# Performance work log

Hardware: AMD Instinct MI355X
Metric: run time of the kernel (lower is better)

The kernel has to match this reference:

```python
import jax, jax.numpy as jnp
import numpy as np

N = 50000        # nodes
E = 400000       # edges (no self-loops; self-loops appended in forward)
IN_DIM = 128
H, C = 4, 64     # heads, channels per head
D = H * C        # 256
NEG_SLOPE = 0.2


def setup_inputs() -> dict:
    key = jax.random.key(0)
    ks = jax.random.split(key, 8)
    x = jax.random.normal(ks[0], (N, IN_DIM), jnp.float32)
    # build edges with no self-loops (src != dst), matching the module's mask
    src = jax.random.randint(ks[1], (E,), 0, N)
    off = jax.random.randint(ks[2], (E,), 1, N)
    dst = (src + off) % N
    edge_index = jnp.stack([src, dst]).astype(jnp.int32)
    inp = {"x": x, "edge_index": edge_index}
    dims_in = [IN_DIM, D, D, D, D]
    for l in range(5):
        k = jax.random.split(ks[3 + l], 4)
        inp[f"W{l}"] = jax.random.normal(k[0], (D, dims_in[l]), jnp.float32) * 0.05
        inp[f"att_src{l}"] = jax.random.normal(k[1], (1, H, C), jnp.float32) * 0.05
        inp[f"att_dst{l}"] = jax.random.normal(k[2], (1, H, C), jnp.float32) * 0.05
        inp[f"bias{l}"] = jnp.zeros((D,), jnp.float32)
    return inp


def _gat_layer(x, W, a_src, a_dst, b, src, dst, relu_out):
    # linear projection, reshape to [N, H, C]
    h = (x @ W.T).reshape(N, H, C)
    alpha_src = jnp.sum(h * a_src, axis=-1)   # [N, H]
    alpha_dst = jnp.sum(h * a_dst, axis=-1)   # [N, H]
    # per-edge logits: alpha_j (source) + alpha_i (dest)
    alpha = jax.nn.leaky_relu(alpha_src[src] + alpha_dst[dst], negative_slope=NEG_SLOPE)  # [E', H]
    # segment softmax over destination neighborhoods (max is detached, as in the original)
    m = jax.lax.stop_gradient(jax.ops.segment_max(alpha, dst, num_segments=N))  # [N, H]
    e = jnp.exp(alpha - m[dst])
    s = jax.ops.segment_sum(e, dst, num_segments=N) + 1e-16
    a = e / s[dst]                                                             # [E', H]
    # weighted scatter-add aggregation of gathered source features
    out = jax.ops.segment_sum(a[:, :, None] * h[src], dst, num_segments=N)     # [N, H, C]
    out = out.reshape(N, D) + b
    return jax.nn.relu(out) if relu_out else out


def reference(x, edge_index,
              W0, att_src0, att_dst0, bias0,
              W1, att_src1, att_dst1, bias1,
              W2, att_src2, att_dst2, bias2,
              W3, att_src3, att_dst3, bias3,
              W4, att_src4, att_dst4, bias4):
    # input edges contain no self-loops; append one self-loop per node (as in the trace)
    loops = jnp.arange(N, dtype=edge_index.dtype)
    src = jnp.concatenate([edge_index[0], loops])
    dst = jnp.concatenate([edge_index[1], loops])
    params = [(W0, att_src0, att_dst0, bias0), (W1, att_src1, att_dst1, bias1),
              (W2, att_src2, att_dst2, bias2), (W3, att_src3, att_dst3, bias3),
              (W4, att_src4, att_dst4, bias4)]
    h = x
    for l, (W, a_s, a_d, b) in enumerate(params):
        h = _gat_layer(h, W, a_s, a_d, b, src, dst, relu_out=(l < 4))
    return h
```

## Files before the change

### kernel.cpp

```cpp
#include <hip/hip_runtime.h>
#include <hip/hip_bf16.h>

#define H 4
#define D 256
#define NEG_SLOPE 0.2f

typedef __attribute__((ext_vector_type(8))) _Float16 f16x8;
typedef __attribute__((ext_vector_type(4))) _Float16 f16x4;
typedef __attribute__((ext_vector_type(4))) float f32x4;

__global__ void k_cvt_all(const float* __restrict__ x,
                          const float* __restrict__ w0, const float* __restrict__ w1,
                          const float* __restrict__ w2, const float* __restrict__ w3,
                          const float* __restrict__ w4,
                          _Float16* __restrict__ xf, _Float16* __restrict__ wf,
                          int nx4) {
    int i = blockIdx.x * blockDim.x + threadIdx.x;
    const int nW0 = 128 * 256 / 4, nW = 256 * 256 / 4;
    const float* src;
    _Float16* dst;
    int off;
    if (i < nx4) { src = x; dst = xf; off = i; }
    else {
        i -= nx4;
        if (i < nW0) { src = w0; dst = wf; off = i; }
        else {
            i -= nW0;
            int l = i / nW, r2 = i % nW;
            if (l >= 4) return;
            const float* ws[4] = {w1, w2, w3, w4};
            src = ws[l];
            dst = wf + 128 * 256 + (size_t)l * 256 * 256;
            off = r2;
        }
    }
    float4 v = ((const float4*)src)[off];
    f16x4 o = {(_Float16)v.x, (_Float16)v.y, (_Float16)v.z, (_Float16)v.w};
    *(f16x4*)&dst[(size_t)off * 4] = o;
}

template<int K>
__global__ __launch_bounds__(256) void k_gemm_mfma(
        const _Float16* __restrict__ xf, const _Float16* __restrict__ wf,
        const float* __restrict__ att_src, const float* __restrict__ att_dst,
        _Float16* __restrict__ hmat, float* __restrict__ alpha_src,
        float* __restrict__ alpha_dst, int nrows) {
    __shared__ _Float16 sx[64][40];
    __shared__ _Float16 sw[256][40];
    int t = threadIdx.x;
    int w = t >> 6, l = t & 63;
    int r = l & 15, q = l >> 4;
    int row0 = blockIdx.x * 64;
    f32x4 acc[16];
    #pragma unroll
    for (int cf = 0; cf < 16; ++cf) acc[cf] = (f32x4){0.f, 0.f, 0.f, 0.f};

    for (int k0 = 0; k0 < K; k0 += 32) {
        __syncthreads();
        {
            int gr = row0 + (t >> 2);
            uint4 v = make_uint4(0, 0, 0, 0);
            if (gr < nrows) v = *(const uint4*)&xf[(size_t)gr * K + k0 + (t & 3) * 8];
            *(uint4*)&sx[t >> 2][(t & 3) * 8] = v;
        }
        #pragma unroll
        for (int i = 0; i < 4; ++i) {
            int wr = (t >> 2) + i * 64;
            uint4 v = *(const uint4*)&wf[(size_t)wr * K + k0 + (t & 3) * 8];
            *(uint4*)&sw[wr][(t & 3) * 8] = v;
        }
        __syncthreads();
        f16x8 a = *(f16x8*)&sx[w * 16 + r][q * 8];
        #pragma unroll
        for (int cf = 0; cf < 16; ++cf) {
            f16x8 b = *(f16x8*)&sw[cf * 16 + r][q * 8];
            acc[cf] = __builtin_amdgcn_mfma_f32_16x16x32_f16(a, b, acc[cf], 0, 0, 0);
        }
    }
    #pragma unroll
    for (int cf = 0; cf < 16; ++cf) {
        #pragma unroll
        for (int i = 0; i < 4; ++i) {
            int gr = row0 + w * 16 + q * 4 + i;
            if (gr < nrows) hmat[(size_t)gr * D + cf * 16 + r] = (_Float16)acc[cf][i];
        }
    }
    float asv[16], adv[16];
    #pragma unroll
    for (int cf = 0; cf < 16; ++cf) {
        asv[cf] = att_src[cf * 16 + r];
        adv[cf] = att_dst[cf * 16 + r];
    }
    #pragma unroll
    for (int i = 0; i < 4; ++i) {
        #pragma unroll
        for (int h4 = 0; h4 < 4; ++h4) {
            float ps = 0.f, pd = 0.f;
            #pragma unroll
            for (int j = 0; j < 4; ++j) {
                int cf = h4 * 4 + j;
                ps += acc[cf][i] * asv[cf];
                pd += acc[cf][i] * adv[cf];
            }
            #pragma unroll
            for (int m = 1; m < 16; m <<= 1) {
                ps += __shfl_xor(ps, m);
                pd += __shfl_xor(pd, m);
            }
            int gr = row0 + w * 16 + q * 4 + i;
            if (r == 0 && gr < nrows) {
                alpha_src[gr * 4 + h4] = ps;
                alpha_dst[gr * 4 + h4] = pd;
            }
        }
    }
}

__global__ void k_deg(const int* __restrict__ ei, int E, int E2, int* __restrict__ deg) {
    int e = blockIdx.x * blockDim.x + threadIdx.x;
    if (e >= E2) return;
    int de = (e < E) ? ei[E + e] : (e - E);
    atomicAdd(&deg[de], 1);
}

__global__ void k_scan_block(const int* __restrict__ deg, int* __restrict__ incl,
                             int* __restrict__ bsum, int n) {
    __shared__ int sd[256];
    int t = threadIdx.x;
    int i = blockIdx.x * 256 + t;
    int v = (i < n) ? deg[i] : 0;
    sd[t] = v;
    __syncthreads();
    for (int off = 1; off < 256; off <<= 1) {
        int add = (t >= off) ? sd[t - off] : 0;
        __syncthreads();
        sd[t] += add;
        __syncthreads();
    }
    if (i < n) incl[i] = sd[t];
    if (t == 255) bsum[blockIdx.x] = sd[255];
}

__global__ void k_scan_bsum(int* __restrict__ bsum, int nb) {
    __shared__ int sd[256];
    int t = threadIdx.x;
    int v = (t < nb) ? bsum[t] : 0;
    sd[t] = v;
    __syncthreads();
    for (int off = 1; off < 256; off <<= 1) {
        int add = (t >= off) ? sd[t - off] : 0;
        __syncthreads();
        sd[t] += add;
        __syncthreads();
    }
    if (t < nb) bsum[t] = sd[t] - v;
}

__global__ void k_rowptr(const int* __restrict__ incl, const int* __restrict__ deg,
                         const int* __restrict__ boff, int* __restrict__ row_ptr,
                         int n, int total) {
    int i = blockIdx.x * blockDim.x + threadIdx.x;
    if (i < n) row_ptr[i] = incl[i] - deg[i] + boff[i >> 8];
    if (i == 0) row_ptr[n] = total;
}

__global__ void k_scatter(const int* __restrict__ ei, int E, int E2,
                          const int* __restrict__ row_ptr, int* __restrict__ cursor,
                          int* __restrict__ csr_src) {
    int e = blockIdx.x * blockDim.x + threadIdx.x;
    if (e >= E2) return;
    int se, de;
    if (e < E) { se = ei[e]; de = ei[E + e]; }
    else       { se = e - E; de = se; }
    int pos = atomicAdd(&cursor[de], 1);
    csr_src[row_ptr[de] + pos] = se;
}

__global__ __launch_bounds__(256) void k_aggregate(const _Float16* __restrict__ hmat,
        const int* __restrict__ row_ptr, const int* __restrict__ csr_src,
        const float* __restrict__ alpha_src, const float* __restrict__ alpha_dst,
        const float* __restrict__ bias, float* __restrict__ outf,
        _Float16* __restrict__ outx, int relu, int nrows) {
    int node = (blockIdx.x * 256 + threadIdx.x) >> 6;
    if (node >= nrows) return;
    int lane = threadIdx.x & 63;
    int e2 = lane >> 5;
    int c  = lane & 31;
    int head = c >> 3;
    int st = row_ptr[node], en = row_ptr[node + 1];
    int deg = en - st;
    float a_d = alpha_dst[node * 4 + head];
    float acc[8] = {};
    float ssum = 0.f;
    for (int b = 0; b < deg; b += 16) {
        int sn[8];
        #pragma unroll
        for (int j = 0; j < 8; ++j) {
            int e = b + e2 * 8 + j;
            int li = st + (e < deg ? e : deg - 1);
            sn[j] = csr_src[li];
        }
        f16x8 hv[8];
        #pragma unroll
        for (int j = 0; j < 8; ++j)
            hv[j] = *(const f16x8*)&hmat[(size_t)sn[j] * D + c * 8];
        float as[8];
        #pragma unroll
        for (int j = 0; j < 8; ++j) as[j] = alpha_src[sn[j] * 4 + head];
        #pragma unroll
        for (int j = 0; j < 8; ++j) {
            int e = b + e2 * 8 + j;
            float a = as[j] + a_d;
            a = a > 0.f ? a : NEG_SLOPE * a;
            float ex = (e < deg) ? __expf(a) : 0.f;
            ssum += ex;
            #pragma unroll
            for (int k = 0; k < 8; ++k) acc[k] += ex * (float)hv[j][k];
        }
    }
    ssum += __shfl_xor(ssum, 32);
    #pragma unroll
    for (int k = 0; k < 8; ++k) acc[k] += __shfl_xor(acc[k], 32);
    if (e2 == 0) {
        float sinv = 1.f / (ssum + 1e-16f);
        float4 b0 = *(const float4*)&bias[c * 8];
        float4 b1 = *(const float4*)&bias[c * 8 + 4];
        float o[8];
        o[0] = acc[0] * sinv + b0.x; o[1] = acc[1] * sinv + b0.y;
        o[2] = acc[2] * sinv + b0.z; o[3] = acc[3] * sinv + b0.w;
        o[4] = acc[4] * sinv + b1.x; o[5] = acc[5] * sinv + b1.y;
        o[6] = acc[6] * sinv + b1.z; o[7] = acc[7] * sinv + b1.w;
        if (relu) {
            #pragma unroll
            for (int k = 0; k < 8; ++k) o[k] = fmaxf(o[k], 0.f);
        }
        if (outx) {
            f16x8 o8 = {(_Float16)o[0], (_Float16)o[1], (_Float16)o[2], (_Float16)o[3],
                        (_Float16)o[4], (_Float16)o[5], (_Float16)o[6], (_Float16)o[7]};
            *(f16x8*)&outx[(size_t)node * D + c * 8] = o8;
        } else {
            *(float4*)&outf[(size_t)node * D + c * 8] =
                make_float4(o[0], o[1], o[2], o[3]);
            *(float4*)&outf[(size_t)node * D + c * 8 + 4] =
                make_float4(o[4], o[5], o[6], o[7]);
        }
    }
}

extern "C" void kernel_launch(void* const* d_in, const int* in_sizes, int n_in,
                              void* d_out, int out_size, void* d_ws, size_t ws_size,
                              hipStream_t stream) {
    const float* x = (const float*)d_in[0];
    const int* ei = (const int*)d_in[1];
    const int N  = in_sizes[0] / 128;
    const int E  = in_sizes[1] / 2;
    const int E2 = E + N;

    char* wsp = (char*)d_ws;
    size_t off = 0;
    auto alloc = [&](size_t bytes) -> void* {
        void* p = wsp + off;
        off += (bytes + 255) & ~(size_t)255;
        return p;
    };
    _Float16* bufH  = (_Float16*)alloc((size_t)N * D * 2);
    _Float16* xf16  = (_Float16*)alloc((size_t)N * D * 2);
    _Float16* wf16  = (_Float16*)alloc((size_t)(128 * 256 + 4 * 256 * 256) * 2);
    float* alpha_src = (float*)alloc((size_t)N * H * 4);
    float* alpha_dst = (float*)alloc((size_t)N * H * 4);
    int*   deg       = (int*)alloc((size_t)N * 4);
    int*   incl      = (int*)alloc((size_t)N * 4);
    int*   bsum      = (int*)alloc(256 * 4);
    int*   row_ptr   = (int*)alloc((size_t)(N + 1) * 4);
    int*   cursor    = (int*)alloc((size_t)N * 4);
    int*   csr_src   = (int*)alloc((size_t)E2 * 4);
    (void)ws_size;

    hipMemsetAsync(deg, 0, (size_t)N * 4, stream);
    hipMemsetAsync(cursor, 0, (size_t)N * 4, stream);

    int nx4 = N * 128 / 4;
    int tot4 = nx4 + 128 * 256 / 4 + 4 * (256 * 256 / 4);
    k_cvt_all<<<(tot4 + 255) / 256, 256, 0, stream>>>(
        x, (const float*)d_in[2], (const float*)d_in[6], (const float*)d_in[10],
        (const float*)d_in[14], (const float*)d_in[18], xf16, wf16, nx4);

    int egrid = (E2 + 255) / 256;
    k_deg<<<egrid, 256, 0, stream>>>(ei, E, E2, deg);
    int nb = (N + 255) / 256;
    k_scan_block<<<nb, 256, 0, stream>>>(deg, incl, bsum, N);
    k_scan_bsum<<<1, 256, 0, stream>>>(bsum, nb);
    k_rowptr<<<nb, 256, 0, stream>>>(incl, deg, bsum, row_ptr, N, E2);
    k_scatter<<<egrid, 256, 0, stream>>>(ei, E, E2, row_ptr, cursor, csr_src);

    int ggrid = (N + 63) / 64;
    int agrid = (N + 3) / 4;
    for (int l = 0; l < 5; ++l) {
        const float* as_ = (const float*)d_in[3 + 4 * l];
        const float* ad_ = (const float*)d_in[4 + 4 * l];
        const float* bs_ = (const float*)d_in[5 + 4 * l];
        const _Float16* wl = (l == 0) ? wf16
                           : wf16 + 128 * 256 + (size_t)(l - 1) * 256 * 256;

        if (l == 0)
            k_gemm_mfma<128><<<ggrid, 256, 0, stream>>>(xf16, wl, as_, ad_,
                                                        bufH, alpha_src, alpha_dst, N);
        else
            k_gemm_mfma<256><<<ggrid, 256, 0, stream>>>(xf16, wl, as_, ad_,
                                                        bufH, alpha_src, alpha_dst, N);

        int last = (l == 4);
        k_aggregate<<<agrid, 256, 0, stream>>>(bufH, row_ptr, csr_src,
                                               alpha_src, alpha_dst, bs_,
                                               last ? (float*)d_out : nullptr,
                                               last ? nullptr : xf16,
                                               last ? 0 : 1, N);
    }
}
```

Baseline: 430.0 us.

## Register-prefetch next K tile and double K step in MFMA projection GEMM

The projection GEMM now stages K in chunks of 64 instead of 32, halving the number of barrier pairs. It also prefetches the next chunk's X and W tiles into registers while the current chunk is being computed, overlapping global loads with MFMA work. The cost is more VGPRs for the prefetch buffers (10 uint4 per thread) and larger LDS tiles, which may reduce occupancy.

```diff
diff --git a/kernel.cpp b/kernel.cpp
--- a/kernel.cpp
+++ b/kernel.cpp
@@ -45,36 +45,64 @@
         const float* __restrict__ att_src, const float* __restrict__ att_dst,
         _Float16* __restrict__ hmat, float* __restrict__ alpha_src,
         float* __restrict__ alpha_dst, int nrows) {
-    __shared__ _Float16 sx[64][40];
-    __shared__ _Float16 sw[256][40];
+    const int NSTEP = K / 64;
+    __shared__ _Float16 sx[64][72];
+    __shared__ _Float16 sw[256][72];
     int t = threadIdx.x;
     int w = t >> 6, l = t & 63;
     int r = l & 15, q = l >> 4;
     int row0 = blockIdx.x * 64;
+    int srow = t >> 2;
+    int scol = (t & 3) * 16;
+    int gxr  = row0 + srow;
+    bool xok = (gxr < nrows);
+
     f32x4 acc[16];
     #pragma unroll
     for (int cf = 0; cf < 16; ++cf) acc[cf] = (f32x4){0.f, 0.f, 0.f, 0.f};
 
-    for (int k0 = 0; k0 < K; k0 += 32) {
-        __syncthreads();
-        {
-            int gr = row0 + (t >> 2);
-            uint4 v = make_uint4(0, 0, 0, 0);
-            if (gr < nrows) v = *(const uint4*)&xf[(size_t)gr * K + k0 + (t & 3) * 8];
-            *(uint4*)&sx[t >> 2][(t & 3) * 8] = v;
-        }
-        #pragma unroll
-        for (int i = 0; i < 4; ++i) {
-            int wr = (t >> 2) + i * 64;
-            uint4 v = *(const uint4*)&wf[(size_t)wr * K + k0 + (t & 3) * 8];
-            *(uint4*)&sw[wr][(t & 3) * 8] = v;
-        }
-        __syncthreads();
-        f16x8 a = *(f16x8*)&sx[w * 16 + r][q * 8];
-        #pragma unroll
-        for (int cf = 0; cf < 16; ++cf) {
-            f16x8 b = *(f16x8*)&sw[cf * 16 + r][q * 8];
-            acc[cf] = __builtin_amdgcn_mfma_f32_16x16x32_f16(a, b, acc[cf], 0, 0, 0);
+    uint4 ldx[2], ldw[8];
+    #pragma unroll
+    for (int u = 0; u < 2; ++u)
+        ldx[u] = xok ? *(const uint4*)&xf[(size_t)gxr * K + scol + u * 8]
+                     : make_uint4(0, 0, 0, 0);
+    #pragma unroll
+    for (int i = 0; i < 4; ++i)
+        #pragma unroll
+        for (int u = 0; u < 2; ++u)
+            ldw[i * 2 + u] = *(const uint4*)&wf[(size_t)(srow + i * 64) * K + scol + u * 8];
+
+    for (int step = 0; step < NSTEP; ++step) {
+        __syncthreads();
+        #pragma unroll
+        for (int u = 0; u < 2; ++u)
+            *(uint4*)&sx[srow][scol + u * 8] = ldx[u];
+        #pragma unroll
+        for (int i = 0; i < 4; ++i)
+            #pragma unroll
+            for (int u = 0; u < 2; ++u)
+                *(uint4*)&sw[srow + i * 64][scol + u * 8] = ldw[i * 2 + u];
+        if (step + 1 < NSTEP) {
+            int k0 = (step + 1) * 64;
+            #pragma unroll
+            for (int u = 0; u < 2; ++u)
+                ldx[u] = xok ? *(const uint4*)&xf[(size_t)gxr * K + k0 + scol + u * 8]
+                             : make_uint4(0, 0, 0, 0);
+            #pragma unroll
+            for (int i = 0; i < 4; ++i)
+                #pragma unroll
+                for (int u = 0; u < 2; ++u)
+                    ldw[i * 2 + u] = *(const uint4*)&wf[(size_t)(srow + i * 64) * K + k0 + scol + u * 8];
+        }
+        __syncthreads();
+        #pragma unroll
+        for (int kk = 0; kk < 2; ++kk) {
+            f16x8 a = *(f16x8*)&sx[w * 16 + r][kk * 32 + q * 8];
+            #pragma unroll
+            for (int cf = 0; cf < 16; ++cf) {
+                f16x8 b = *(f16x8*)&sw[cf * 16 + r][kk * 32 + q * 8];
+                acc[cf] = __builtin_amdgcn_mfma_f32_16x16x32_f16(a, b, acc[cf], 0, 0, 0);
+            }
         }
     }
     #pragma unroll
```

Result: slower. 527.6 us (+22.7%).

## Pre-swizzle weights into MFMA fragment layout and split GEMM columns across blocks

Applied to the files above, without the earlier changes.

Weights are converted once into an MFMA B-fragment order, so each GEMM block copies its half of W into shared memory with one contiguous load and no per-k-step syncs. The A operand is loaded straight from global into registers for the whole K range. The grid gains a second dimension that splits the 256 output columns into two halves of 128, so each half computes the attention logits for two heads. This drops the per-k-tile shared staging and barriers and doubles the number of blocks. The cost is that A is read twice from global memory, more registers are used, and the single conversion kernel becomes six launches.

```diff
diff --git a/kernel.cpp b/kernel.cpp
--- a/kernel.cpp
+++ b/kernel.cpp
@@ -9,96 +9,103 @@
 typedef __attribute__((ext_vector_type(4))) _Float16 f16x4;
 typedef __attribute__((ext_vector_type(4))) float f32x4;
 
-__global__ void k_cvt_all(const float* __restrict__ x,
-                          const float* __restrict__ w0, const float* __restrict__ w1,
-                          const float* __restrict__ w2, const float* __restrict__ w3,
-                          const float* __restrict__ w4,
-                          _Float16* __restrict__ xf, _Float16* __restrict__ wf,
-                          int nx4) {
+__global__ void k_cvt(const float* __restrict__ in, _Float16* __restrict__ out, int n4) {
     int i = blockIdx.x * blockDim.x + threadIdx.x;
-    const int nW0 = 128 * 256 / 4, nW = 256 * 256 / 4;
-    const float* src;
-    _Float16* dst;
-    int off;
-    if (i < nx4) { src = x; dst = xf; off = i; }
-    else {
-        i -= nx4;
-        if (i < nW0) { src = w0; dst = wf; off = i; }
-        else {
-            i -= nW0;
-            int l = i / nW, r2 = i % nW;
-            if (l >= 4) return;
-            const float* ws[4] = {w1, w2, w3, w4};
-            src = ws[l];
-            dst = wf + 128 * 256 + (size_t)l * 256 * 256;
-            off = r2;
-        }
-    }
-    float4 v = ((const float4*)src)[off];
+    if (i >= n4) return;
+    float4 v = ((const float4*)in)[i];
     f16x4 o = {(_Float16)v.x, (_Float16)v.y, (_Float16)v.z, (_Float16)v.w};
-    *(f16x4*)&dst[(size_t)off * 4] = o;
+    *(f16x4*)&out[(size_t)i * 4] = o;
+}
+
+template<int K>
+__global__ void k_cvt_wfrag(const float* __restrict__ W, _Float16* __restrict__ wfrag) {
+    const int NKS = K / 32;
+    int idx = blockIdx.x * blockDim.x + threadIdx.x;
+    if (idx >= 16 * NKS * 64) return;
+    int l  = idx & 63;
+    int ks = (idx >> 6) % NKS;
+    int c16 = idx / (NKS * 64);
+    int col = c16 * 16 + (l & 15);
+    int k0  = ks * 32 + (l >> 4) * 8;
+    const float* src = &W[(size_t)col * K + k0];
+    float4 v0 = *(const float4*)src;
+    float4 v1 = *(const float4*)(src + 4);
+    f16x8 o = {(_Float16)v0.x, (_Float16)v0.y, (_Float16)v0.z, (_Float16)v0.w,
+               (_Float16)v1.x, (_Float16)v1.y, (_Float16)v1.z, (_Float16)v1.w};
+    *(f16x8*)&wfrag[(size_t)idx * 8] = o;
 }
 
 template<int K>
 __global__ __launch_bounds__(256) void k_gemm_mfma(
-        const _Float16* __restrict__ xf, const _Float16* __restrict__ wf,
+        const _Float16* __restrict__ xf, const _Float16* __restrict__ wfrag,
         const float* __restrict__ att_src, const float* __restrict__ att_dst,
         _Float16* __restrict__ hmat, float* __restrict__ alpha_src,
         float* __restrict__ alpha_dst, int nrows) {
-    __shared__ _Float16 sx[64][40];
-    __shared__ _Float16 sw[256][40];
+    const int NKS = K / 32;
+    __shared__ _Float16 sw[8 * NKS * 64 * 8];
     int t = threadIdx.x;
     int w = t >> 6, l = t & 63;
     int r = l & 15, q = l >> 4;
-    int row0 = blockIdx.x * 64;
-    f32x4 acc[16];
-    #pragma unroll
-    for (int cf = 0; cf < 16; ++cf) acc[cf] = (f32x4){0.f, 0.f, 0.f, 0.f};
-
-    for (int k0 = 0; k0 < K; k0 += 32) {
-        __syncthreads();
-        {
-            int gr = row0 + (t >> 2);
-            uint4 v = make_uint4(0, 0, 0, 0);
-            if (gr < nrows) v = *(const uint4*)&xf[(size_t)gr * K + k0 + (t & 3) * 8];
-            *(uint4*)&sx[t >> 2][(t & 3) * 8] = v;
-        }
-        #pragma unroll
-        for (int i = 0; i < 4; ++i) {
-            int wr = (t >> 2) + i * 64;
-            uint4 v = *(const uint4*)&wf[(size_t)wr * K + k0 + (t & 3) * 8];
-            *(uint4*)&sw[wr][(t & 3) * 8] = v;
-        }
-        __syncthreads();
-        f16x8 a = *(f16x8*)&sx[w * 16 + r][q * 8];
-        #pragma unroll
-        for (int cf = 0; cf < 16; ++cf) {
-            f16x8 b = *(f16x8*)&sw[cf * 16 + r][q * 8];
-            acc[cf] = __builtin_amdgcn_mfma_f32_16x16x32_f16(a, b, acc[cf], 0, 0, 0);
-        }
-    }
-    #pragma unroll
-    for (int cf = 0; cf < 16; ++cf) {
+    int row0  = blockIdx.x * 64;
+    int split = blockIdx.y;
+
+    {
+        const uint4* wsrc = (const uint4*)(wfrag + (size_t)split * 8 * NKS * 64 * 8);
+        uint4* wdst = (uint4*)sw;
+        const int nchunk = 8 * NKS * 64;
+        #pragma unroll
+        for (int i = 0; i < nchunk / 256; ++i)
+            wdst[i * 256 + t] = wsrc[i * 256 + t];
+    }
+
+    int gr_a = row0 + w * 16 + r;
+    bool aok = (gr_a < nrows);
+    f16x8 a[NKS];
+    #pragma unroll
+    for (int ks = 0; ks < NKS; ++ks) {
+        if (aok) a[ks] = *(const f16x8*)&xf[(size_t)gr_a * K + ks * 32 + q * 8];
+        else     a[ks] = (f16x8){0, 0, 0, 0, 0, 0, 0, 0};
+    }
+
+    __syncthreads();
+
+    f32x4 acc[8];
+    #pragma unroll
+    for (int cf = 0; cf < 8; ++cf) acc[cf] = (f32x4){0.f, 0.f, 0.f, 0.f};
+    #pragma unroll
+    for (int cf = 0; cf < 8; ++cf) {
+        f16x8 b[NKS];
+        #pragma unroll
+        for (int ks = 0; ks < NKS; ++ks)
+            b[ks] = *(f16x8*)&sw[(size_t)((cf * NKS + ks) * 64 + l) * 8];
+        #pragma unroll
+        for (int ks = 0; ks < NKS; ++ks)
+            acc[cf] = __builtin_amdgcn_mfma_f32_16x16x32_f16(a[ks], b[ks], acc[cf], 0, 0, 0);
+    }
+
+    #pragma unroll
+    for (int cf = 0; cf < 8; ++cf) {
         #pragma unroll
         for (int i = 0; i < 4; ++i) {
             int gr = row0 + w * 16 + q * 4 + i;
-            if (gr < nrows) hmat[(size_t)gr * D + cf * 16 + r] = (_Float16)acc[cf][i];
-        }
-    }
-    float asv[16], adv[16];
-    #pragma unroll
-    for (int cf = 0; cf < 16; ++cf) {
-        asv[cf] = att_src[cf * 16 + r];
-        adv[cf] = att_dst[cf * 16 + r];
+            if (gr < nrows)
+                hmat[(size_t)gr * D + split * 128 + cf * 16 + r] = (_Float16)acc[cf][i];
+        }
+    }
+    float asv[8], adv[8];
+    #pragma unroll
+    for (int cf = 0; cf < 8; ++cf) {
+        asv[cf] = att_src[split * 128 + cf * 16 + r];
+        adv[cf] = att_dst[split * 128 + cf * 16 + r];
     }
     #pragma unroll
     for (int i = 0; i < 4; ++i) {
         #pragma unroll
-        for (int h4 = 0; h4 < 4; ++h4) {
+        for (int hh = 0; hh < 2; ++hh) {
             float ps = 0.f, pd = 0.f;
             #pragma unroll
             for (int j = 0; j < 4; ++j) {
-                int cf = h4 * 4 + j;
+                int cf = hh * 4 + j;
                 ps += acc[cf][i] * asv[cf];
                 pd += acc[cf][i] * adv[cf];
             }
@@ -109,8 +116,8 @@
             }
             int gr = row0 + w * 16 + q * 4 + i;
             if (r == 0 && gr < nrows) {
-                alpha_src[gr * 4 + h4] = ps;
-                alpha_dst[gr * 4 + h4] = pd;
+                alpha_src[gr * 4 + split * 2 + hh] = ps;
+                alpha_dst[gr * 4 + split * 2 + hh] = pd;
             }
         }
     }
@@ -265,7 +272,7 @@
     };
     _Float16* bufH  = (_Float16*)alloc((size_t)N * D * 2);
     _Float16* xf16  = (_Float16*)alloc((size_t)N * D * 2);
-    _Float16* wf16  = (_Float16*)alloc((size_t)(128 * 256 + 4 * 256 * 256) * 2);
+    _Float16* wfrag = (_Float16*)alloc((size_t)(128 * 256 + 4 * 256 * 256) * 2);
     float* alpha_src = (float*)alloc((size_t)N * H * 4);
     float* alpha_dst = (float*)alloc((size_t)N * H * 4);
     int*   deg       = (int*)alloc((size_t)N * 4);
@@ -280,10 +287,13 @@
     hipMemsetAsync(cursor, 0, (size_t)N * 4, stream);
 
     int nx4 = N * 128 / 4;
-    int tot4 = nx4 + 128 * 256 / 4 + 4 * (256 * 256 / 4);
-    k_cvt_all<<<(tot4 + 255) / 256, 256, 0, stream>>>(
-        x, (const float*)d_in[2], (const float*)d_in[6], (const float*)d_in[10],
-        (const float*)d_in[14], (const float*)d_in[18], xf16, wf16, nx4);
+    k_cvt<<<(nx4 + 255) / 256, 256, 0, stream>>>(x, xf16, nx4);
+    k_cvt_wfrag<128><<<(16 * 4 * 64 + 255) / 256, 256, 0, stream>>>(
+        (const float*)d_in[2], wfrag);
+    for (int l = 1; l < 5; ++l)
+        k_cvt_wfrag<256><<<(16 * 8 * 64 + 255) / 256, 256, 0, stream>>>(
+            (const float*)d_in[2 + 4 * l],
+            wfrag + 128 * 256 + (size_t)(l - 1) * 256 * 256);
 
     int egrid = (E2 + 255) / 256;
     k_deg<<<egrid, 256, 0, stream>>>(ei, E, E2, deg);
@@ -293,14 +303,14 @@
     k_rowptr<<<nb, 256, 0, stream>>>(incl, deg, bsum, row_ptr, N, E2);
     k_scatter<<<egrid, 256, 0, stream>>>(ei, E, E2, row_ptr, cursor, csr_src);
 
-    int ggrid = (N + 63) / 64;
+    dim3 ggrid((N + 63) / 64, 2);
     int agrid = (N + 3) / 4;
     for (int l = 0; l < 5; ++l) {
         const float* as_ = (const float*)d_in[3 + 4 * l];
         const float* ad_ = (const float*)d_in[4 + 4 * l];
         const float* bs_ = (const float*)d_in[5 + 4 * l];
-        const _Float16* wl = (l == 0) ? wf16
-                           : wf16 + 128 * 256 + (size_t)(l - 1) * 256 * 256;
+        const _Float16* wl = (l == 0) ? wfrag
+                           : wfrag + 128 * 256 + (size_t)(l - 1) * 256 * 256;
 
         if (l == 0)
             k_gemm_mfma<128><<<ggrid, 256, 0, stream>>>(xf16, wl, as_, ad_,
```

New measurement: 423.4 us. About the same (-1.5%).
